# Kernel optimization log

Measured on AMD Instinct MI355X. Metric: run time of the kernel, lower is better.

The kernel has to match this reference:

```python
import jax, jax.numpy as jnp
import numpy as np

N_NODES = 100000


def setup_inputs() -> dict:
    key = jax.random.key(0)
    ks = jax.random.split(key, 8)
    IN, HID, OUT = 128, 128, 64
    E = 1600000
    x = jax.random.normal(ks[0], (N_NODES, IN), dtype=jnp.float32)
    edge_index = jax.random.randint(ks[1], (2, E), 0, N_NODES, dtype=jnp.int64)
    # PyG SAGEConv params: lin_l (applied to aggregated neighbors, with bias),
    # lin_r (root weight, no bias).
    def lin(k, fi, fo):
        return jax.random.normal(k, (fi, fo), dtype=jnp.float32) / np.sqrt(fi)
    Wl0 = lin(ks[2], IN, HID)
    bl0 = jnp.zeros((HID,), dtype=jnp.float32)
    Wr0 = lin(ks[3], IN, HID)
    Wl1 = lin(ks[4], HID, OUT)
    bl1 = jnp.zeros((OUT,), dtype=jnp.float32)
    Wr1 = lin(ks[5], HID, OUT)
    return {"x": x, "edge_index": edge_index,
            "Wl0": Wl0, "bl0": bl0, "Wr0": Wr0,
            "Wl1": Wl1, "bl1": bl1, "Wr1": Wr1}


def _sage_conv(h, src, dst, Wl, bl, Wr):
    # mean aggregation of source features onto target nodes
    summed = jax.ops.segment_sum(h[src], dst, num_segments=N_NODES)  # [N, d]
    cnt = jax.ops.segment_sum(jnp.ones((src.shape[0], 1), h.dtype), dst,
                              num_segments=N_NODES)                  # [N, 1]
    agg = summed / jnp.maximum(cnt, 1.0)
    return agg @ Wl + bl + h @ Wr


def reference(x, edge_index, Wl0, bl0, Wr0, Wl1, bl1, Wr1):
    src, dst = edge_index[0], edge_index[1]
    h = jax.nn.relu(_sage_conv(x, src, dst, Wl0, bl0, Wr0))
    # dropout is identity in eval mode (training=False)
    return _sage_conv(h, src, dst, Wl1, bl1, Wr1)
```

## Files before the change

kernel.cpp:

```cpp
#include <hip/hip_runtime.h>


typedef short short8 __attribute__((ext_vector_type(8)));
typedef float f32x4 __attribute__((ext_vector_type(4)));
typedef float f32x2 __attribute__((ext_vector_type(2)));

#define NBUCK 782
#define BCAP  3072
#define EPB   8192

static __device__ __forceinline__ unsigned short f2bf(float f) {
    union { float f; unsigned u; } c; c.f = f;
    unsigned u = c.u + 0x7fffu + ((c.u >> 16) & 1u);
    return (unsigned short)(u >> 16);
}
static __device__ __forceinline__ float bf2f(unsigned short b) {
    union { unsigned u; float f; } c; c.u = ((unsigned)b) << 16;
    return c.f;
}
static __device__ __forceinline__ float bf2f_s(short b) {
    return bf2f((unsigned short)b);
}

static __device__ __forceinline__ unsigned char f2fp8(float x) {
    union { float f; unsigned u; } c; c.f = x;
    unsigned s = (c.u >> 24) & 0x80u;
    float a = __builtin_fabsf(x);
    if (a < 0.015625f) {
        int m = (int)rintf(a * 512.0f);
        return (unsigned char)(s | (unsigned)m);
    }
    unsigned u = c.u + 0x7ffffu + ((c.u >> 20) & 1u);
    int e = (int)((u >> 23) & 0xff) - 120;
    unsigned m = (u >> 20) & 7u;
    if (e > 15) { e = 15; m = 6; }
    return (unsigned char)(s | (unsigned)(e << 3) | m);
}

static __device__ __forceinline__ void acc_fp8x4(unsigned w, float* a) {
#if __has_builtin(__builtin_amdgcn_cvt_pk_f32_fp8)
    f32x2 lo = __builtin_amdgcn_cvt_pk_f32_fp8((int)w, false);
    f32x2 hi = __builtin_amdgcn_cvt_pk_f32_fp8((int)w, true);
    a[0] += lo[0]; a[1] += lo[1]; a[2] += hi[0]; a[3] += hi[1];
#else
    #pragma unroll
    for (int j = 0; j < 4; ++j) {
        unsigned b = (w >> (8 * j)) & 0xffu;
        union { unsigned u; float f; } c;
        c.u = ((b & 0x80u) << 24) | ((b & 0x7fu) << 20);
        a[j] += c.f * 0x1p120f;
    }
#endif
}
static __device__ __forceinline__ void acc_row16(uint4 w, float* a) {
    acc_fp8x4(w.x, a + 0);  acc_fp8x4(w.y, a + 4);
    acc_fp8x4(w.z, a + 8);  acc_fp8x4(w.w, a + 12);
}

__global__ __launch_bounds__(256) void k_pack2(const float* __restrict__ Wl0,
        const float* __restrict__ Wr0, const float* __restrict__ Wl1,
        const float* __restrict__ Wr1, unsigned short* __restrict__ Wp0,
        unsigned short* __restrict__ Wp1) {
    int tid = blockIdx.x * 256 + threadIdx.x;
    const float *WA, *WB; int CA; unsigned short* Wp;
    if (tid < 4096) {
        WA = Wl0; WB = Wr0; CA = 128; Wp = Wp0;
    } else {
        tid -= 4096;
        if (tid >= 2048) return;
        WA = Wl1; WB = Wr1; CA = 64; Wp = Wp1;
    }
    int lane = tid & 63, kk = (tid >> 6) & 3, tg = tid >> 8;
    int l15 = lane & 15, quad = lane >> 4;
    int c = tg * 16 + l15;
    const float* W = (c < CA) ? WA : WB;
    int cc = (c < CA) ? c : c - CA;
    short8 v;
    #pragma unroll
    for (int j = 0; j < 8; ++j) {
        int k = kk * 32 + quad * 8 + j;
        v[j] = (short)f2bf(W[(size_t)k * CA + cc]);
    }
    *(short8*)(Wp + (size_t)tid * 8) = v;
}

__global__ __launch_bounds__(256) void k_gemm0_bucket(
        const float* __restrict__ X, const unsigned short* __restrict__ Wp,
        unsigned char* __restrict__ P0, unsigned short* __restrict__ Q0, int Nrows,
        const int* __restrict__ src, const int* __restrict__ dst,
        int* __restrict__ cursor, int* __restrict__ bregion,
        int E, int bucketBlocks) {
    const int t = threadIdx.x;
    if ((int)blockIdx.x >= bucketBlocks) {
        const int wave = t >> 6, lane = t & 63;
        const int quad = lane >> 4, l15 = lane & 15;
        const int row0 = (blockIdx.x - bucketBlocks) * 32;
        const int c0w = wave * 64;
        f32x4 acc[2][4];
        #pragma unroll
        for (int mt = 0; mt < 2; ++mt)
            #pragma unroll
            for (int tt = 0; tt < 4; ++tt) acc[mt][tt] = (f32x4){0.f, 0.f, 0.f, 0.f};
        #pragma unroll
        for (int kk = 0; kk < 4; ++kk) {
            const int k0 = kk * 32 + quad * 8;
            short8 a[2];
            #pragma unroll
            for (int mt = 0; mt < 2; ++mt) {
                int row = row0 + mt * 16 + l15;
                if (row > Nrows - 1) row = Nrows - 1;
                const float* xp = X + (size_t)row * 128 + k0;
                float4 f0 = *(const float4*)xp;
                float4 f1 = *(const float4*)(xp + 4);
                short8 v;
                v[0] = (short)f2bf(f0.x); v[1] = (short)f2bf(f0.y);
                v[2] = (short)f2bf(f0.z); v[3] = (short)f2bf(f0.w);
                v[4] = (short)f2bf(f1.x); v[5] = (short)f2bf(f1.y);
                v[6] = (short)f2bf(f1.z); v[7] = (short)f2bf(f1.w);
                a[mt] = v;
            }
            short8 b[4];
            #pragma unroll
            for (int tt = 0; tt < 4; ++tt) {
                int tg = (c0w >> 4) + tt;
                b[tt] = *(const short8*)(Wp + ((size_t)(tg * 4 + kk) * 64 + lane) * 8);
            }
            #pragma unroll
            for (int mt = 0; mt < 2; ++mt)
                #pragma unroll
                for (int tt = 0; tt < 4; ++tt)
                    acc[mt][tt] = __builtin_amdgcn_mfma_f32_16x16x32_bf16(
                        a[mt], b[tt], acc[mt][tt], 0, 0, 0);
        }
        #pragma unroll
        for (int mt = 0; mt < 2; ++mt)
            #pragma unroll
            for (int r = 0; r < 4; ++r) {
                int row = row0 + mt * 16 + quad * 4 + r;
                if (row < Nrows) {
                    if (c0w < 128) {
                        #pragma unroll
                        for (int tt = 0; tt < 4; ++tt)
                            P0[(size_t)row * 128 + c0w + tt * 16 + l15] =
                                f2fp8(acc[mt][tt][r]);
                    } else {
                        #pragma unroll
                        for (int tt = 0; tt < 4; ++tt)
                            Q0[(size_t)row * 128 + (c0w - 128) + tt * 16 + l15] =
                                f2bf(acc[mt][tt][r]);
                    }
                }
            }
        return;
    }
    __shared__ int hist[NBUCK];
    __shared__ int basel[NBUCK];
    int bid = blockIdx.x;
    for (int i = t; i < NBUCK; i += 256) hist[i] = 0;
    __syncthreads();
    int e0 = bid * EPB + t * 32;
    if (e0 + 32 <= E) {
        #pragma unroll
        for (int q = 0; q < 8; ++q) {
            int4 v = *(const int4*)(dst + e0 + q * 4);
            atomicAdd(&hist[v.x >> 7], 1);
            atomicAdd(&hist[v.y >> 7], 1);
            atomicAdd(&hist[v.z >> 7], 1);
            atomicAdd(&hist[v.w >> 7], 1);
        }
    } else {
        for (int j = 0; j < 32; ++j)
            if (e0 + j < E) atomicAdd(&hist[dst[e0 + j] >> 7], 1);
    }
    __syncthreads();
    for (int i = t; i < NBUCK; i += 256) {
        int c = hist[i];
        basel[i] = (c > 0) ? atomicAdd(&cursor[i], c) : 0;
    }
    __syncthreads();
    for (int i = t; i < NBUCK; i += 256) hist[i] = 0;
    __syncthreads();
    if (e0 + 32 <= E) {
        #pragma unroll
        for (int q = 0; q < 8; ++q) {
            int4 dv = *(const int4*)(dst + e0 + q * 4);
            int4 sv = *(const int4*)(src + e0 + q * 4);
            int dd[4] = {dv.x, dv.y, dv.z, dv.w};
            int ss[4] = {sv.x, sv.y, sv.z, sv.w};
            #pragma unroll
            for (int j = 0; j < 4; ++j) {
                int b = dd[j] >> 7;
                int r = atomicAdd(&hist[b], 1);
                bregion[(size_t)b * BCAP + basel[b] + r] = ss[j] | ((dd[j] & 127) << 20);
            }
        }
    } else {
        for (int j = 0; j < 32; ++j) {
            if (e0 + j < E) {
                int dd = dst[e0 + j], ss = src[e0 + j];
                int b = dd >> 7;
                int r = atomicAdd(&hist[b], 1);
                bregion[(size_t)b * BCAP + basel[b] + r] = ss | ((dd & 127) << 20);
            }
        }
    }
}

__global__ __launch_bounds__(256) void k_csr(const int* __restrict__ cursor,
                                             const int* __restrict__ bregion,
                                             int* __restrict__ rowptr,
                                             int* __restrict__ csr, int Nn) {
    __shared__ int words[BCAP];
    __shared__ int hist[128], sc[128], rank[128];
    __shared__ int red[256];
    int b = blockIdx.x, t = threadIdx.x;
    int part = 0;
    for (int i = t; i < b; i += 256) part += cursor[i];
    red[t] = part;
    if (t < 128) { hist[t] = 0; rank[t] = 0; }
    __syncthreads();
    #pragma unroll
    for (int off = 128; off > 0; off >>= 1) {
        if (t < off) red[t] += red[t + off];
        __syncthreads();
    }
    int gbase = red[0];
    int cnt = cursor[b];
    for (int i = t; i < cnt; i += 256) {
        int w = bregion[(size_t)b * BCAP + i];
        words[i] = w;
        atomicAdd(&hist[w >> 20], 1);
    }
    __syncthreads();
    if (t < 128) sc[t] = hist[t];
    __syncthreads();
    #pragma unroll
    for (int off = 1; off < 128; off <<= 1) {
        int x = 0;
        if (t < 128 && t >= off) x = sc[t - off];
        __syncthreads();
        if (t < 128) sc[t] += x;
        __syncthreads();
    }
    if (t < 128) sc[t] -= hist[t];
    __syncthreads();
    if (t < 128) {
        int node = b * 128 + t;
        if (node <= Nn) rowptr[node] = gbase + sc[t];
    }
    for (int i = t; i < cnt; i += 256) {
        int w = words[i];
        int d7 = w >> 20;
        int r = atomicAdd(&rank[d7], 1);
        csr[gbase + sc[d7] + r] = w & 0xFFFFF;
    }
}

__global__ __launch_bounds__(256) void k_gemm1(const unsigned short* __restrict__ Xv,
                                               const unsigned short* __restrict__ Wp,
                                               unsigned char* __restrict__ P1,
                                               unsigned short* __restrict__ Q1,
                                               int Nrows) {
    const int t = threadIdx.x;
    const int wave = t >> 6, lane = t & 63;
    const int quad = lane >> 4, l15 = lane & 15;
    const int row0 = blockIdx.x * 32;
    const int c0w = wave * 32;
    f32x4 acc[2][2];
    #pragma unroll
    for (int mt = 0; mt < 2; ++mt)
        #pragma unroll
        for (int tt = 0; tt < 2; ++tt) acc[mt][tt] = (f32x4){0.f, 0.f, 0.f, 0.f};
    #pragma unroll
    for (int kk = 0; kk < 4; ++kk) {
        const int k0 = kk * 32 + quad * 8;
        short8 a[2];
        #pragma unroll
        for (int mt = 0; mt < 2; ++mt) {
            int row = row0 + mt * 16 + l15;
            if (row > Nrows - 1) row = Nrows - 1;
            a[mt] = *(const short8*)(Xv + (size_t)row * 128 + k0);
        }
        short8 b[2];
        #pragma unroll
        for (int tt = 0; tt < 2; ++tt) {
            int tg = (c0w >> 4) + tt;
            b[tt] = *(const short8*)(Wp + ((size_t)(tg * 4 + kk) * 64 + lane) * 8);
        }
        #pragma unroll
        for (int mt = 0; mt < 2; ++mt)
            #pragma unroll
            for (int tt = 0; tt < 2; ++tt)
                acc[mt][tt] = __builtin_amdgcn_mfma_f32_16x16x32_bf16(
                    a[mt], b[tt], acc[mt][tt], 0, 0, 0);
    }
    #pragma unroll
    for (int mt = 0; mt < 2; ++mt)
        #pragma unroll
        for (int r = 0; r < 4; ++r) {
            int row = row0 + mt * 16 + quad * 4 + r;
            if (row < Nrows) {
                if (c0w < 64) {
                    #pragma unroll
                    for (int tt = 0; tt < 2; ++tt)
                        P1[(size_t)row * 64 + c0w + tt * 16 + l15] =
                            f2fp8(acc[mt][tt][r]);
                } else {
                    #pragma unroll
                    for (int tt = 0; tt < 2; ++tt)
                        Q1[(size_t)row * 64 + (c0w - 64) + tt * 16 + l15] =
                            f2bf(acc[mt][tt][r]);
                }
            }
        }
}

__global__ __launch_bounds__(256) void k_agg0(const unsigned char* __restrict__ P0,
                                              const unsigned short* __restrict__ Q0,
                                              const int* __restrict__ rowptr,
                                              const int* __restrict__ csr,
                                              const float* __restrict__ bl0,
                                              unsigned short* __restrict__ h, int Nn) {
    int wave = threadIdx.x >> 6, lane = threadIdx.x & 63;
    int g = lane >> 3, l7 = lane & 7;
    int n = (blockIdx.x * 4 + wave) * 8 + g;
    bool live = (n < Nn);
    int st = 0, dg = 0;
    if (live) { st = rowptr[n]; dg = rowptr[n + 1] - st; }
    float acc[16] = {};
    int e = 0;
    for (; e + 2 <= dg; e += 2) {
        int s0 = csr[st + e];
        int s1 = csr[st + e + 1];
        uint4 w0 = *(const uint4*)(P0 + (size_t)s0 * 128 + l7 * 16);
        uint4 w1 = *(const uint4*)(P0 + (size_t)s1 * 128 + l7 * 16);
        acc_row16(w0, acc);
        acc_row16(w1, acc);
    }
    if (e < dg) {
        int s0 = csr[st + e];
        uint4 w0 = *(const uint4*)(P0 + (size_t)s0 * 128 + l7 * 16);
        acc_row16(w0, acc);
    }
    if (live) {
        float inv = 1.f / fmaxf((float)dg, 1.f);
        short8 q0 = *(const short8*)(Q0 + (size_t)n * 128 + l7 * 16);
        short8 q1 = *(const short8*)(Q0 + (size_t)n * 128 + l7 * 16 + 8);
        float bb[16];
        *(float4*)(bb + 0)  = *(const float4*)(bl0 + l7 * 16);
        *(float4*)(bb + 4)  = *(const float4*)(bl0 + l7 * 16 + 4);
        *(float4*)(bb + 8)  = *(const float4*)(bl0 + l7 * 16 + 8);
        *(float4*)(bb + 12) = *(const float4*)(bl0 + l7 * 16 + 12);
        short8 o0, o1;
        #pragma unroll
        for (int j = 0; j < 8; ++j)
            o0[j] = (short)f2bf(fmaxf(acc[j] * inv + bb[j] + bf2f_s(q0[j]), 0.f));
        #pragma unroll
        for (int j = 0; j < 8; ++j)
            o1[j] = (short)f2bf(fmaxf(acc[8 + j] * inv + bb[8 + j] + bf2f_s(q1[j]), 0.f));
        *(short8*)(h + (size_t)n * 128 + l7 * 16) = o0;
        *(short8*)(h + (size_t)n * 128 + l7 * 16 + 8) = o1;
    }
}

__global__ __launch_bounds__(256) void k_agg1(const unsigned char* __restrict__ P1,
                                              const unsigned short* __restrict__ Q1,
                                              const int* __restrict__ rowptr,
                                              const int* __restrict__ csr,
                                              const float* __restrict__ bl1,
                                              float* __restrict__ out, int Nn) {
    int wave = threadIdx.x >> 6, lane = threadIdx.x & 63;
    int g = lane >> 2, l3 = lane & 3;
    int n = (blockIdx.x * 4 + wave) * 16 + g;
    bool live = (n < Nn);
    int st = 0, dg = 0;
    if (live) { st = rowptr[n]; dg = rowptr[n + 1] - st; }
    float acc[16] = {};
    int e = 0;
    for (; e + 2 <= dg; e += 2) {
        int s0 = csr[st + e];
        int s1 = csr[st + e + 1];
        uint4 w0 = *(const uint4*)(P1 + (size_t)s0 * 64 + l3 * 16);
        uint4 w1 = *(const uint4*)(P1 + (size_t)s1 * 64 + l3 * 16);
        acc_row16(w0, acc);
        acc_row16(w1, acc);
    }
    if (e < dg) {
        int s0 = csr[st + e];
        uint4 w0 = *(const uint4*)(P1 + (size_t)s0 * 64 + l3 * 16);
        acc_row16(w0, acc);
    }
    if (live) {
        float inv = 1.f / fmaxf((float)dg, 1.f);
        short8 q0 = *(const short8*)(Q1 + (size_t)n * 64 + l3 * 16);
        short8 q1 = *(const short8*)(Q1 + (size_t)n * 64 + l3 * 16 + 8);
        float bb[16];
        *(float4*)(bb + 0)  = *(const float4*)(bl1 + l3 * 16);
        *(float4*)(bb + 4)  = *(const float4*)(bl1 + l3 * 16 + 4);
        *(float4*)(bb + 8)  = *(const float4*)(bl1 + l3 * 16 + 8);
        *(float4*)(bb + 12) = *(const float4*)(bl1 + l3 * 16 + 12);
        float4 o[4];
        #pragma unroll
        for (int j = 0; j < 8; ++j)
            ((float*)o)[j] = acc[j] * inv + bb[j] + bf2f_s(q0[j]);
        #pragma unroll
        for (int j = 0; j < 8; ++j)
            ((float*)o)[8 + j] = acc[8 + j] * inv + bb[8 + j] + bf2f_s(q1[j]);
        #pragma unroll
        for (int q = 0; q < 4; ++q)
            *(float4*)(out + (size_t)n * 64 + l3 * 16 + q * 4) = o[q];
    }
}

extern "C" void kernel_launch(void* const* d_in, const int* in_sizes, int n_in,
                              void* d_out, int out_size, void* d_ws, size_t ws_size,
                              hipStream_t stream) {
    const float* x   = (const float*)d_in[0];
    const int* eidx  = (const int*)d_in[1];
    const float* Wl0 = (const float*)d_in[2];
    const float* bl0 = (const float*)d_in[3];
    const float* Wr0 = (const float*)d_in[4];
    const float* Wl1 = (const float*)d_in[5];
    const float* bl1 = (const float*)d_in[6];
    const float* Wr1 = (const float*)d_in[7];
    float* out = (float*)d_out;

    const int N = in_sizes[0] / 128;
    const int E = in_sizes[1] / 2;
    const int* src = eidx;
    const int* dst = eidx + E;

    int* rowptr  = (int*)d_ws;
    int* cursor  = rowptr + (N + 4);
    int* bregion = cursor + 784;
    int* csr     = bregion + (size_t)NBUCK * BCAP;
    unsigned short* Wp0 = (unsigned short*)(csr + E);
    unsigned short* Wp1 = Wp0 + 32768;
    unsigned char*  P0  = (unsigned char*)(Wp1 + 16384);
    unsigned short* Q0  = (unsigned short*)(P0 + (size_t)N * 128);
    unsigned short* h   = Q0 + (size_t)N * 128;
    unsigned char*  P1  = (unsigned char*)(h + (size_t)N * 128);
    unsigned short* Q1  = (unsigned short*)(P1 + (size_t)N * 64);

    hipMemsetAsync(cursor, 0, NBUCK * sizeof(int), stream);

    k_pack2<<<24, 256, 0, stream>>>(Wl0, Wr0, Wl1, Wr1, Wp0, Wp1);

    int gemmBlocks = (N + 31) / 32;
    int nbb = (E + EPB - 1) / EPB;
    k_gemm0_bucket<<<gemmBlocks + nbb, 256, 0, stream>>>(
        x, Wp0, P0, Q0, N, src, dst, cursor, bregion, E, nbb);
    k_csr<<<NBUCK, 256, 0, stream>>>(cursor, bregion, rowptr, csr, N);

    k_agg0<<<(N + 31) / 32, 256, 0, stream>>>(P0, Q0, rowptr, csr, bl0, h, N);
    k_gemm1<<<(N + 31) / 32, 256, 0, stream>>>(h, Wp1, P1, Q1, N);
    k_agg1<<<(N + 63) / 64, 256, 0, stream>>>(P1, Q1, rowptr, csr, bl1, out, N);
}
```

Baseline: 296.6 us.

## Fuse layer-0 aggregation with layer-1 GEMM via swizzled LDS tile; shrink bucket chunk

The layer-0 mean aggregation and the layer-1 projection GEMM now run in one kernel. Each block aggregates 32 nodes, writes the bf16 hidden rows into an XOR-swizzled shared-memory tile, and feeds MFMA directly from LDS. This removes the global write and re-read of the hidden activation h and one kernel launch. Separately, the bucketing pass now handles 2048 edges per block instead of 8192, giving four times as many blocks but more global cursor atomics.

Result: slower. 305.0 us (+2.8%).

```diff
diff --git a/kernel.cpp b/kernel.cpp
--- a/kernel.cpp
+++ b/kernel.cpp
@@ -7,7 +7,7 @@
 
 #define NBUCK 782
 #define BCAP  3072
-#define EPB   8192
+#define EPB   2048
 
 static __device__ __forceinline__ unsigned short f2bf(float f) {
     union { float f; unsigned u; } c; c.f = f;
@@ -158,10 +158,10 @@
     int bid = blockIdx.x;
     for (int i = t; i < NBUCK; i += 256) hist[i] = 0;
     __syncthreads();
-    int e0 = bid * EPB + t * 32;
-    if (e0 + 32 <= E) {
-        #pragma unroll
-        for (int q = 0; q < 8; ++q) {
+    int e0 = bid * EPB + t * 8;
+    if (e0 + 8 <= E) {
+        #pragma unroll
+        for (int q = 0; q < 2; ++q) {
             int4 v = *(const int4*)(dst + e0 + q * 4);
             atomicAdd(&hist[v.x >> 7], 1);
             atomicAdd(&hist[v.y >> 7], 1);
@@ -169,7 +169,7 @@
             atomicAdd(&hist[v.w >> 7], 1);
         }
     } else {
-        for (int j = 0; j < 32; ++j)
+        for (int j = 0; j < 8; ++j)
             if (e0 + j < E) atomicAdd(&hist[dst[e0 + j] >> 7], 1);
     }
     __syncthreads();
@@ -180,9 +180,9 @@
     __syncthreads();
     for (int i = t; i < NBUCK; i += 256) hist[i] = 0;
     __syncthreads();
-    if (e0 + 32 <= E) {
-        #pragma unroll
-        for (int q = 0; q < 8; ++q) {
+    if (e0 + 8 <= E) {
+        #pragma unroll
+        for (int q = 0; q < 2; ++q) {
             int4 dv = *(const int4*)(dst + e0 + q * 4);
             int4 sv = *(const int4*)(src + e0 + q * 4);
             int dd[4] = {dv.x, dv.y, dv.z, dv.w};
@@ -195,7 +195,7 @@
             }
         }
     } else {
-        for (int j = 0; j < 32; ++j) {
+        for (int j = 0; j < 8; ++j) {
             if (e0 + j < E) {
                 int dd = dst[e0 + j], ss = src[e0 + j];
                 int b = dd >> 7;
@@ -256,13 +256,62 @@
     }
 }
 
-__global__ __launch_bounds__(256) void k_gemm1(const unsigned short* __restrict__ Xv,
-                                               const unsigned short* __restrict__ Wp,
-                                               unsigned char* __restrict__ P1,
-                                               unsigned short* __restrict__ Q1,
-                                               int Nrows) {
+__global__ __launch_bounds__(256) void k_agg0_gemm1(
+        const unsigned char* __restrict__ P0,
+        const unsigned short* __restrict__ Q0,
+        const int* __restrict__ rowptr, const int* __restrict__ csr,
+        const float* __restrict__ bl0,
+        const unsigned short* __restrict__ Wp,
+        unsigned char* __restrict__ P1, unsigned short* __restrict__ Q1,
+        int Nn) {
+    __shared__ unsigned short ht[32 * 128];
     const int t = threadIdx.x;
     const int wave = t >> 6, lane = t & 63;
+    {
+        int g = lane >> 3, l7 = lane & 7;
+        int nloc = wave * 8 + g;
+        int n = blockIdx.x * 32 + nloc;
+        bool live = (n < Nn);
+        int st = 0, dg = 0;
+        if (live) { st = rowptr[n]; dg = rowptr[n + 1] - st; }
+        float acc[16] = {};
+        int e = 0;
+        for (; e + 2 <= dg; e += 2) {
+            int s0 = csr[st + e];
+            int s1 = csr[st + e + 1];
+            uint4 w0 = *(const uint4*)(P0 + (size_t)s0 * 128 + l7 * 16);
+            uint4 w1 = *(const uint4*)(P0 + (size_t)s1 * 128 + l7 * 16);
+            acc_row16(w0, acc);
+            acc_row16(w1, acc);
+        }
+        if (e < dg) {
+            int s0 = csr[st + e];
+            uint4 w0 = *(const uint4*)(P0 + (size_t)s0 * 128 + l7 * 16);
+            acc_row16(w0, acc);
+        }
+        short8 o0 = (short8){0,0,0,0,0,0,0,0}, o1 = o0;
+        if (live) {
+            float inv = 1.f / fmaxf((float)dg, 1.f);
+            short8 q0 = *(const short8*)(Q0 + (size_t)n * 128 + l7 * 16);
+            short8 q1 = *(const short8*)(Q0 + (size_t)n * 128 + l7 * 16 + 8);
+            float bb[16];
+            *(float4*)(bb + 0)  = *(const float4*)(bl0 + l7 * 16);
+            *(float4*)(bb + 4)  = *(const float4*)(bl0 + l7 * 16 + 4);
+            *(float4*)(bb + 8)  = *(const float4*)(bl0 + l7 * 16 + 8);
+            *(float4*)(bb + 12) = *(const float4*)(bl0 + l7 * 16 + 12);
+            #pragma unroll
+            for (int j = 0; j < 8; ++j)
+                o0[j] = (short)f2bf(fmaxf(acc[j] * inv + bb[j] + bf2f_s(q0[j]), 0.f));
+            #pragma unroll
+            for (int j = 0; j < 8; ++j)
+                o1[j] = (short)f2bf(fmaxf(acc[8 + j] * inv + bb[8 + j] + bf2f_s(q1[j]), 0.f));
+        }
+        unsigned sw = (unsigned)(nloc & 7) << 4;
+        char* base = (char*)ht + nloc * 256;
+        *(short8*)(base + (((unsigned)(l7 * 32)) ^ sw)) = o0;
+        *(short8*)(base + (((unsigned)(l7 * 32 + 16)) ^ sw)) = o1;
+    }
+    __syncthreads();
     const int quad = lane >> 4, l15 = lane & 15;
     const int row0 = blockIdx.x * 32;
     const int c0w = wave * 32;
@@ -273,13 +322,13 @@
         for (int tt = 0; tt < 2; ++tt) acc[mt][tt] = (f32x4){0.f, 0.f, 0.f, 0.f};
     #pragma unroll
     for (int kk = 0; kk < 4; ++kk) {
-        const int k0 = kk * 32 + quad * 8;
         short8 a[2];
         #pragma unroll
         for (int mt = 0; mt < 2; ++mt) {
-            int row = row0 + mt * 16 + l15;
-            if (row > Nrows - 1) row = Nrows - 1;
-            a[mt] = *(const short8*)(Xv + (size_t)row * 128 + k0);
+            int row = mt * 16 + l15;
+            const char* p = (const char*)ht + row * 256 +
+                (((unsigned)(kk * 64 + quad * 16)) ^ ((unsigned)(row & 7) << 4));
+            a[mt] = *(const short8*)p;
         }
         short8 b[2];
         #pragma unroll
@@ -299,7 +348,7 @@
         #pragma unroll
         for (int r = 0; r < 4; ++r) {
             int row = row0 + mt * 16 + quad * 4 + r;
-            if (row < Nrows) {
+            if (row < Nn) {
                 if (c0w < 64) {
                     #pragma unroll
                     for (int tt = 0; tt < 2; ++tt)
@@ -313,54 +362,6 @@
                 }
             }
         }
-}
-
-__global__ __launch_bounds__(256) void k_agg0(const unsigned char* __restrict__ P0,
-                                              const unsigned short* __restrict__ Q0,
-                                              const int* __restrict__ rowptr,
-                                              const int* __restrict__ csr,
-                                              const float* __restrict__ bl0,
-                                              unsigned short* __restrict__ h, int Nn) {
-    int wave = threadIdx.x >> 6, lane = threadIdx.x & 63;
-    int g = lane >> 3, l7 = lane & 7;
-    int n = (blockIdx.x * 4 + wave) * 8 + g;
-    bool live = (n < Nn);
-    int st = 0, dg = 0;
-    if (live) { st = rowptr[n]; dg = rowptr[n + 1] - st; }
-    float acc[16] = {};
-    int e = 0;
-    for (; e + 2 <= dg; e += 2) {
-        int s0 = csr[st + e];
-        int s1 = csr[st + e + 1];
-        uint4 w0 = *(const uint4*)(P0 + (size_t)s0 * 128 + l7 * 16);
-        uint4 w1 = *(const uint4*)(P0 + (size_t)s1 * 128 + l7 * 16);
-        acc_row16(w0, acc);
-        acc_row16(w1, acc);
-    }
-    if (e < dg) {
-        int s0 = csr[st + e];
-        uint4 w0 = *(const uint4*)(P0 + (size_t)s0 * 128 + l7 * 16);
-        acc_row16(w0, acc);
-    }
-    if (live) {
-        float inv = 1.f / fmaxf((float)dg, 1.f);
-        short8 q0 = *(const short8*)(Q0 + (size_t)n * 128 + l7 * 16);
-        short8 q1 = *(const short8*)(Q0 + (size_t)n * 128 + l7 * 16 + 8);
-        float bb[16];
-        *(float4*)(bb + 0)  = *(const float4*)(bl0 + l7 * 16);
-        *(float4*)(bb + 4)  = *(const float4*)(bl0 + l7 * 16 + 4);
-        *(float4*)(bb + 8)  = *(const float4*)(bl0 + l7 * 16 + 8);
-        *(float4*)(bb + 12) = *(const float4*)(bl0 + l7 * 16 + 12);
-        short8 o0, o1;
-        #pragma unroll
-        for (int j = 0; j < 8; ++j)
-            o0[j] = (short)f2bf(fmaxf(acc[j] * inv + bb[j] + bf2f_s(q0[j]), 0.f));
-        #pragma unroll
-        for (int j = 0; j < 8; ++j)
-            o1[j] = (short)f2bf(fmaxf(acc[8 + j] * inv + bb[8 + j] + bf2f_s(q1[j]), 0.f));
-        *(short8*)(h + (size_t)n * 128 + l7 * 16) = o0;
-        *(short8*)(h + (size_t)n * 128 + l7 * 16 + 8) = o1;
-    }
 }
 
 __global__ __launch_bounds__(256) void k_agg1(const unsigned char* __restrict__ P1,
@@ -452,7 +453,7 @@
         x, Wp0, P0, Q0, N, src, dst, cursor, bregion, E, nbb);
     k_csr<<<NBUCK, 256, 0, stream>>>(cursor, bregion, rowptr, csr, N);
 
-    k_agg0<<<(N + 31) / 32, 256, 0, stream>>>(P0, Q0, rowptr, csr, bl0, h, N);
-    k_gemm1<<<(N + 31) / 32, 256, 0, stream>>>(h, Wp1, P1, Q1, N);
+    k_agg0_gemm1<<<(N + 31) / 32, 256, 0, stream>>>(
+        P0, Q0, rowptr, csr, bl0, Wp1, P1, Q1, N);
     k_agg1<<<(N + 63) / 64, 256, 0, stream>>>(P1, Q1, rowptr, csr, bl1, out, N);
 }
```
